# Performance work log

Measured on AMD Instinct MI355X. Metric: run time of the kernel, lower is better.

Reference implementation:

```python
import jax, jax.numpy as jnp
import numpy as np

GRID_RES_SAMPLE = 0.08  # config.grid_resolution_sample
VOXEL_SIZE = 0.04       # scene voxel size encoded in transforms


def setup_inputs() -> dict:
    key = jax.random.key(0)
    ks = jax.random.split(key, 4)
    B, X = 4, 96
    G = 192            # == ceil(X * GRID_RES_SAMPLE / VOXEL_SIZE), matches dynamic size_voxel_grid
    N = 500_000        # sparse occupied voxels per scene
    NUM_ADD = 5000     # static stand-in for occ_grids.sum()+100 mask augmentations
    # scene voxel-grid transform: scale VOXEL_SIZE, translate -5m (same structure per scene)
    T = np.eye(4, dtype=np.float32)
    T[0, 0] = T[1, 1] = T[2, 2] = VOXEL_SIZE
    T[:3, 3] = -5.0
    transforms = np.tile(T, (B, 1, 1)).astype(np.float32)
    transforms_inv = np.stack([np.linalg.inv(t) for t in transforms]).astype(np.float32)
    # per-batch regular coordinate grids with random world offsets in [0,1)m
    offs = np.asarray(jax.random.uniform(ks[0], (B, 3), dtype=jnp.float32))
    ax = np.arange(X, dtype=np.float32) * GRID_RES_SAMPLE
    gx, gy, gz = np.meshgrid(ax, ax, ax, indexing='ij')
    base = np.stack([gx, gy, gz], axis=0)  # [3,X,X,X]
    coords = (base[None] + offs[:, :, None, None, None]).astype(np.float32)
    sparse = jax.random.randint(ks[1], (B, N, 3), 0, 400, dtype=jnp.int32)
    rand_idx = jax.random.randint(ks[2], (3, NUM_ADD), 0, X, dtype=jnp.int32)
    conv_w = jnp.ones((1, 1, 5, 5, 5), jnp.float32)  # Conv3d(1,1,5) all-ones, no bias
    return {
        'coordinate_grids': jnp.asarray(coords),
        'transforms': jnp.asarray(transforms),
        'transforms_inv': jnp.asarray(transforms_inv),
        'sparse_encoding': sparse,
        'conv_w': conv_w,
        'rand_idx': rand_idx,
        'grid_size': G,
    }


def reference(coordinate_grids, transforms, transforms_inv, sparse_encoding, conv_w, rand_idx, grid_size):
    B, C, X, Y, Z = coordinate_grids.shape
    flat = coordinate_grids.reshape(B, 3, -1)
    min_loc = flat.min(-1)   # [B,3]
    max_loc = flat.max(-1)   # [B,3]
    max_size_grid = (max_loc + GRID_RES_SAMPLE - min_loc).max(0)  # [3]
    min_homo = jnp.concatenate([min_loc, jnp.ones((B, 1), flat.dtype)], axis=1)
    min_voxel_idx = jnp.floor(jnp.einsum('bij,bj->bi', transforms_inv, min_homo)[:, :3])
    min_voxel_idx = jnp.maximum(min_voxel_idx, 0.0)  # [B,3]
    size_vox = jnp.ceil(jnp.einsum('bij,j->bi', transforms_inv[:, :3, :3], max_size_grid).max(0))  # [3], == grid_size
    # shift sparse indices into the local window and filter out-of-range ones
    se = sparse_encoding.astype(jnp.float32) - min_voxel_idx[:, None, :]   # [B,N,3]
    valid = ((se >= 0) & (se < size_vox)).all(-1)                          # [B,N]
    sei = jnp.clip(se.astype(jnp.int32), 0, grid_size - 1)
    occ = jnp.zeros((B, grid_size, grid_size, grid_size), jnp.float32)
    b_idx = jnp.broadcast_to(jnp.arange(B)[:, None], valid.shape)
    occ = occ.at[b_idx, sei[..., 0], sei[..., 1], sei[..., 2]].max(valid.astype(jnp.float32))
    # world position of voxel (0,0,0) of the local window and window extent
    min_homo_idx = jnp.concatenate([min_voxel_idx, jnp.ones((B, 1), flat.dtype)], axis=1)
    pos_base = jnp.einsum('bij,bj->bi', transforms, min_homo_idx)[:, :3]   # [B,3]
    extent = jnp.einsum('bij,j->bi', transforms[:, :3, :3], size_vox)      # [B,3]
    voxel_size = extent / size_vox                                          # [B,3]
    # trilinear interpolation of dense occ grid at the coordinate grid (voxel-center convention)
    p = (coordinate_grids - pos_base[:, :, None, None, None]) / voxel_size[:, :, None, None, None] - 0.5
    p0 = jnp.floor(p)
    f = p - p0                       # [B,3,X,Y,Z]
    p0 = p0.astype(jnp.int32)
    bb = jnp.arange(B)[:, None, None, None]
    out = jnp.zeros((B, X, Y, Z), jnp.float32)
    for dx in (0, 1):
        for dy in (0, 1):
            for dz in (0, 1):
                ix = jnp.clip(p0[:, 0] + dx, 0, grid_size - 1)
                iy = jnp.clip(p0[:, 1] + dy, 0, grid_size - 1)
                iz = jnp.clip(p0[:, 2] + dz, 0, grid_size - 1)
                w = ((f[:, 0] if dx else 1 - f[:, 0]) *
                     (f[:, 1] if dy else 1 - f[:, 1]) *
                     (f[:, 2] if dz else 1 - f[:, 2]))
                out = out + w * occ[bb, ix, iy, iz]
    occ_grids = out[:, None]  # [B,1,X,Y,Z]
    # 5x5x5 all-ones conv mask
    conv = jax.lax.conv_general_dilated(
        occ_grids, conv_w, window_strides=(1, 1, 1),
        padding=[(2, 2), (2, 2), (2, 2)],
        dimension_numbers=('NCDHW', 'OIDHW', 'NCDHW'))
    mask = conv > 0
    # random-index mask augmentation (num_voxels_to_add fixed statically)
    num_add = rand_idx.shape[1]
    badd = jnp.arange(num_add) % B
    mask = mask.at[badd, 0, rand_idx[0], rand_idx[1], rand_idx[2]].set(True)
    return occ_grids.astype(bool), mask
```

## Files before the change

kernel.cpp:

```cpp
#include <hip/hip_runtime.h>
#include <math.h>

#define GS   192
#define XS   96
#define XS3  (XS*XS*XS)
#define GRS  0.08f

#define PI_OFF     256
#define PF_OFF     (256 + 1152*4)
#define OCC_OFF    16384
#define OCC_WORDS  (4*GS*GS*(GS/32))
#define OUT_OFF    (OCC_OFF + OCC_WORDS*4)
#define OUTB_WORDS (4*XS*XS*(XS/32))

__device__ __forceinline__ int clampi(int v, int lo, int hi) {
    return v < lo ? lo : (v > hi ? hi : v);
}

__global__ void k_scalars(const float* __restrict__ coords,
                          const float* __restrict__ T,
                          const float* __restrict__ Tinv,
                          float* ws, int B) {
    __shared__ int imn[12], imx[12];
    __shared__ float SS[64];
    int t = threadIdx.x;
    if (t < 12) { imn[t] = 0x7F800000; imx[t] = 0; }
    __syncthreads();
    int tot = B * 3 * XS;
    for (int e = t; e < tot; e += 256) {
        int b = e / (3 * XS); int c = (e / XS) % 3; int i = e % XS;
        size_t off = (size_t)(b*3 + c) * XS3
                   + (c == 0 ? (size_t)i * XS * XS : (c == 1 ? (size_t)i * XS : (size_t)i));
        int v = __float_as_int(coords[off]);
        atomicMin(&imn[b*3 + c], v);
        atomicMax(&imx[b*3 + c], v);
    }
    __syncthreads();
    if (t == 0) {
        float mnl[12], mxl[12];
        for (int k = 0; k < 12; k++) { mnl[k] = __int_as_float(imn[k]); mxl[k] = __int_as_float(imx[k]); }
        float msg[3];
        for (int c = 0; c < 3; c++) {
            float m = -__builtin_inff();
            for (int b = 0; b < B; b++) {
                float v = __fadd_rn(mxl[b*3 + c], GRS);
                v = __fsub_rn(v, mnl[b*3 + c]);
                m = fmaxf(m, v);
            }
            msg[c] = m;
        }
        for (int b = 0; b < B; b++)
            for (int i = 0; i < 3; i++) {
                const float* R = Tinv + b*16 + i*4;
                float v = __fmul_rn(R[0], mnl[b*3 + 0]);
                v = __fadd_rn(v, __fmul_rn(R[1], mnl[b*3 + 1]));
                v = __fadd_rn(v, __fmul_rn(R[2], mnl[b*3 + 2]));
                v = __fadd_rn(v, R[3]);
                SS[24 + b*3 + i] = fmaxf(floorf(v), 0.0f);
            }
        for (int i = 0; i < 3; i++) {
            float m = -__builtin_inff();
            for (int b = 0; b < B; b++) {
                const float* R = Tinv + b*16 + i*4;
                float v = __fmul_rn(R[0], msg[0]);
                v = __fadd_rn(v, __fmul_rn(R[1], msg[1]));
                v = __fadd_rn(v, __fmul_rn(R[2], msg[2]));
                m = fmaxf(m, v);
            }
            SS[36 + i] = ceilf(m);
        }
        for (int b = 0; b < B; b++)
            for (int i = 0; i < 3; i++) {
                const float* R = T + b*16 + i*4;
                float v = __fmul_rn(R[0], SS[24 + b*3 + 0]);
                v = __fadd_rn(v, __fmul_rn(R[1], SS[24 + b*3 + 1]));
                v = __fadd_rn(v, __fmul_rn(R[2], SS[24 + b*3 + 2]));
                v = __fadd_rn(v, R[3]);
                SS[40 + b*3 + i] = v;
            }
        for (int b = 0; b < B; b++)
            for (int i = 0; i < 3; i++) {
                const float* R = T + b*16 + i*4;
                float v = __fmul_rn(R[0], SS[36 + 0]);
                v = __fadd_rn(v, __fmul_rn(R[1], SS[36 + 1]));
                v = __fadd_rn(v, __fmul_rn(R[2], SS[36 + 2]));
                SS[52 + b*3 + i] = v / SS[36 + i];
            }
        for (int k = 24; k < 64; k++) ws[k] = SS[k];
    }
    __syncthreads();
    int* PI = (int*)((char*)ws + PI_OFF);
    float* PF = (float*)((char*)ws + PF_OFF);
    for (int e = t; e < tot; e += 256) {
        int b = e / (3 * XS); int c = (e / XS) % 3; int i = e % XS;
        size_t off = (size_t)(b*3 + c) * XS3
                   + (c == 0 ? (size_t)i * XS * XS : (c == 1 ? (size_t)i * XS : (size_t)i));
        float v = coords[off];
        float p = (v - SS[40 + b*3 + c]) / SS[52 + b*3 + c] - 0.5f;
        float p0 = floorf(p);
        PI[e] = (int)p0;
        PF[e] = p - p0;
    }
}

__global__ void k_scatter(const int* __restrict__ sparse, const float* __restrict__ ws,
                          unsigned* __restrict__ occ, int N, int total) {
    int t = blockIdx.x * blockDim.x + threadIdx.x;
    if (t >= total) return;
    int b = t / N;
    const float* S = ws;
    int s0 = sparse[(size_t)t*3 + 0];
    int s1 = sparse[(size_t)t*3 + 1];
    int s2 = sparse[(size_t)t*3 + 2];
    float e0 = (float)s0 - S[24 + b*3 + 0];
    float e1 = (float)s1 - S[24 + b*3 + 1];
    float e2 = (float)s2 - S[24 + b*3 + 2];
    if (e0 >= 0.f && e0 < S[36+0] && e1 >= 0.f && e1 < S[36+1] && e2 >= 0.f && e2 < S[36+2]) {
        int x = clampi((int)e0, 0, GS-1);
        int y = clampi((int)e1, 0, GS-1);
        int z = clampi((int)e2, 0, GS-1);
        atomicOr(&occ[(((size_t)b*GS + x)*GS + y)*(GS/32) + (z >> 5)], 1u << (z & 31));
    }
}

__global__ __launch_bounds__(256) void k_interp(const float* __restrict__ ws,
                                                const unsigned* __restrict__ occ,
                                                int* __restrict__ out0,
                                                unsigned* __restrict__ outb,
                                                int total) {
    int gid = blockIdx.x * 256 + threadIdx.x;
    if (gid >= total) return;
    int z = gid % XS;
    int r1 = gid / XS;
    int y = r1 % XS;
    int r2 = r1 / XS;
    int x = r2 % XS;
    int b = r2 / XS;
    const int* PI = (const int*)((const char*)ws + PI_OFF);
    const float* PF = (const float*)((const char*)ws + PF_OFF);
    int ix = PI[(b*3 + 0)*XS + x]; float fx = PF[(b*3 + 0)*XS + x];
    int iy = PI[(b*3 + 1)*XS + y]; float fy = PF[(b*3 + 1)*XS + y];
    int iz = PI[(b*3 + 2)*XS + z]; float fz = PF[(b*3 + 2)*XS + z];
    int x0 = clampi(ix,   0, GS-1), x1 = clampi(ix+1, 0, GS-1);
    int y0 = clampi(iy,   0, GS-1), y1 = clampi(iy+1, 0, GS-1);
    int z0 = clampi(iz,   0, GS-1), z1 = clampi(iz+1, 0, GS-1);
    float wx0 = 1.f - fx, wx1 = fx, wy0 = 1.f - fy, wy1 = fy, wz0 = 1.f - fz, wz1 = fz;
    const unsigned* r00 = occ + (((size_t)b*GS + x0)*GS + y0)*(GS/32);
    const unsigned* r01 = occ + (((size_t)b*GS + x0)*GS + y1)*(GS/32);
    const unsigned* r10 = occ + (((size_t)b*GS + x1)*GS + y0)*(GS/32);
    const unsigned* r11 = occ + (((size_t)b*GS + x1)*GS + y1)*(GS/32);
    float w00 = wx0*wy0, w01 = wx0*wy1, w10 = wx1*wy0, w11 = wx1*wy1;
    float s = 0.f;
    s += w00*wz0*(float)((r00[z0>>5] >> (z0&31)) & 1u);
    s += w00*wz1*(float)((r00[z1>>5] >> (z1&31)) & 1u);
    s += w01*wz0*(float)((r01[z0>>5] >> (z0&31)) & 1u);
    s += w01*wz1*(float)((r01[z1>>5] >> (z1&31)) & 1u);
    s += w10*wz0*(float)((r10[z0>>5] >> (z0&31)) & 1u);
    s += w10*wz1*(float)((r10[z1>>5] >> (z1&31)) & 1u);
    s += w11*wz0*(float)((r11[z0>>5] >> (z0&31)) & 1u);
    s += w11*wz1*(float)((r11[z1>>5] >> (z1&31)) & 1u);
    bool nz = (s != 0.f);
    out0[gid] = nz ? 1 : 0;
    unsigned long long m = __ballot(nz);
    int lane = threadIdx.x & 63;
    if (lane == 0)  outb[gid >> 5] = (unsigned)m;
    if (lane == 32) outb[gid >> 5] = (unsigned)(m >> 32);
}

__global__ __launch_bounds__(256) void k_dilate_bits(const unsigned* __restrict__ outb,
                                                     unsigned* __restrict__ outb2,
                                                     int totalW) {
    int t = blockIdx.x * 256 + threadIdx.x;
    if (t >= totalW) return;
    int w = t % 3;
    int r1 = t / 3;
    int j = r1 % XS;
    int r2 = r1 / XS;
    int i = r2 % XS;
    int b = r2 / XS;
    unsigned accP = 0, accC = 0, accN = 0;
    for (int di = -2; di <= 2; di++) {
        int ii = i + di; if (ii < 0 || ii >= XS) continue;
        for (int dj = -2; dj <= 2; dj++) {
            int jj = j + dj; if (jj < 0 || jj >= XS) continue;
            const unsigned* row = outb + ((size_t)(b*XS + ii)*XS + jj)*3;
            accC |= row[w];
            if (w > 0) accP |= row[w-1];
            if (w < 2) accN |= row[w+1];
        }
    }
    unsigned d = accC
               | (accC << 1) | (accP >> 31)
               | (accC << 2) | (accP >> 30)
               | (accC >> 1) | (accN << 31)
               | (accC >> 2) | (accN << 30);
    outb2[t] = d;
}

__global__ __launch_bounds__(256) void k_expand(const unsigned* __restrict__ outb2,
                                                int* __restrict__ out1, int total) {
    int gid = blockIdx.x * 256 + threadIdx.x;
    if (gid >= total) return;
    out1[gid] = (int)((outb2[gid >> 5] >> (gid & 31)) & 1u);
}

__global__ void k_rand(const int* __restrict__ rand_idx, int* __restrict__ maskout,
                       int nadd, int B) {
    int i = blockIdx.x * blockDim.x + threadIdx.x;
    if (i >= nadd) return;
    int b = i % B;
    int r0 = rand_idx[i], r1 = rand_idx[nadd + i], r2 = rand_idx[2*nadd + i];
    maskout[((size_t)(b*XS + r0)*XS + r1)*XS + r2] = 1;
}

extern "C" void kernel_launch(void* const* d_in, const int* in_sizes, int n_in,
                              void* d_out, int out_size, void* d_ws, size_t ws_size,
                              hipStream_t stream) {
    const float* coords = (const float*)d_in[0];
    const float* T      = (const float*)d_in[1];
    const float* Tinv   = (const float*)d_in[2];
    const int*   sparse = (const int*)d_in[3];
    const int*   rand_i = (const int*)d_in[5];
    int* out = (int*)d_out;

    int B = in_sizes[1] / 16;
    int N = in_sizes[3] / (B * 3);
    int nadd = in_sizes[5] / 3;

    float*    ws    = (float*)d_ws;
    unsigned* occ   = (unsigned*)((char*)d_ws + OCC_OFF);
    unsigned* outb  = (unsigned*)((char*)d_ws + OUT_OFF);
    unsigned* outb2 = (unsigned*)((char*)d_ws + OCC_OFF);
    size_t half = (size_t)B * XS3;

    hipMemsetAsync((char*)d_ws + OCC_OFF, 0, (size_t)OCC_WORDS * 4, stream);

    k_scalars<<<1, 256, 0, stream>>>(coords, T, Tinv, ws, B);
    int totalPts = B * N;
    k_scatter<<<(totalPts + 255) / 256, 256, 0, stream>>>(sparse, ws, occ, N, totalPts);
    int total = B * XS3;
    k_interp<<<(total + 255) / 256, 256, 0, stream>>>(ws, occ, out, outb, total);
    int totalW = B * XS * XS * 3;
    k_dilate_bits<<<(totalW + 255) / 256, 256, 0, stream>>>(outb, outb2, totalW);
    k_expand<<<(total + 255) / 256, 256, 0, stream>>>(outb2, out + half, total);
    k_rand<<<(nadd + 255) / 256, 256, 0, stream>>>(rand_i, out + half, nadd, B);
}
```

Baseline: 153.8 us.

## Fuse dilation, expansion and random-mask scatter into one kernel via bitmask

The random-index augmentation is now built as a bitmask by atomicOr inside the single-block scalar kernel, and that bitmask is ORed into the dilated words. Dilation and expansion to int output are fused into one kernel that stages each block's 256 words in LDS and writes its 8192 ints with a coalesced loop. This drops two kernel launches and the intermediate bit buffer round trip through global memory. In exchange the serial rand loop lands on one block, and the grid now assumes totalW is an exact multiple of 256.

New measurement: 161.1 us. +4.8%, slower.

```diff
diff --git a/kernel.cpp b/kernel.cpp
--- a/kernel.cpp
+++ b/kernel.cpp
@@ -10,8 +10,9 @@
 #define PF_OFF     (256 + 1152*4)
 #define OCC_OFF    16384
 #define OCC_WORDS  (4*GS*GS*(GS/32))
-#define OUT_OFF    (OCC_OFF + OCC_WORDS*4)
 #define OUTB_WORDS (4*XS*XS*(XS/32))
+#define RAND_OFF   (OCC_OFF + OCC_WORDS*4)
+#define OUT_OFF    (RAND_OFF + OUTB_WORDS*4)
 
 __device__ __forceinline__ int clampi(int v, int lo, int hi) {
     return v < lo ? lo : (v > hi ? hi : v);
@@ -20,10 +21,19 @@
 __global__ void k_scalars(const float* __restrict__ coords,
                           const float* __restrict__ T,
                           const float* __restrict__ Tinv,
-                          float* ws, int B) {
+                          float* ws,
+                          const int* __restrict__ rand_idx,
+                          unsigned* __restrict__ randb,
+                          int B, int nadd) {
     __shared__ int imn[12], imx[12];
     __shared__ float SS[64];
     int t = threadIdx.x;
+    for (int idx = t; idx < nadd; idx += 256) {
+        int b = idx % B;
+        int r0 = rand_idx[idx], r1 = rand_idx[nadd + idx], r2 = rand_idx[2*nadd + idx];
+        int e = ((b*XS + r0)*XS + r1)*XS + r2;
+        atomicOr(&randb[e >> 5], 1u << (e & 31));
+    }
     if (t < 12) { imn[t] = 0x7F800000; imx[t] = 0; }
     __syncthreads();
     int tot = B * 3 * XS;
@@ -167,11 +177,10 @@
     if (lane == 32) outb[gid >> 5] = (unsigned)(m >> 32);
 }
 
-__global__ __launch_bounds__(256) void k_dilate_bits(const unsigned* __restrict__ outb,
-                                                     unsigned* __restrict__ outb2,
-                                                     int totalW) {
+__global__ __launch_bounds__(256) void k_dilate_expand(const unsigned* __restrict__ outb,
+                                                       const unsigned* __restrict__ randb,
+                                                       int* __restrict__ out1) {
     int t = blockIdx.x * 256 + threadIdx.x;
-    if (t >= totalW) return;
     int w = t % 3;
     int r1 = t / 3;
     int j = r1 % XS;
@@ -194,23 +203,16 @@
                | (accC << 2) | (accP >> 30)
                | (accC >> 1) | (accN << 31)
                | (accC >> 2) | (accN << 30);
-    outb2[t] = d;
-}
-
-__global__ __launch_bounds__(256) void k_expand(const unsigned* __restrict__ outb2,
-                                                int* __restrict__ out1, int total) {
-    int gid = blockIdx.x * 256 + threadIdx.x;
-    if (gid >= total) return;
-    out1[gid] = (int)((outb2[gid >> 5] >> (gid & 31)) & 1u);
-}
-
-__global__ void k_rand(const int* __restrict__ rand_idx, int* __restrict__ maskout,
-                       int nadd, int B) {
-    int i = blockIdx.x * blockDim.x + threadIdx.x;
-    if (i >= nadd) return;
-    int b = i % B;
-    int r0 = rand_idx[i], r1 = rand_idx[nadd + i], r2 = rand_idx[2*nadd + i];
-    maskout[((size_t)(b*XS + r0)*XS + r1)*XS + r2] = 1;
+    d |= randb[t];
+    __shared__ unsigned lds[256];
+    lds[threadIdx.x] = d;
+    __syncthreads();
+    size_t base = (size_t)blockIdx.x * 8192;
+    #pragma unroll
+    for (int k = 0; k < 32; k++) {
+        int e = k * 256 + threadIdx.x;
+        out1[base + e] = (int)((lds[e >> 5] >> (e & 31)) & 1u);
+    }
 }
 
 extern "C" void kernel_launch(void* const* d_in, const int* in_sizes, int n_in,
@@ -229,19 +231,17 @@
 
     float*    ws    = (float*)d_ws;
     unsigned* occ   = (unsigned*)((char*)d_ws + OCC_OFF);
+    unsigned* randb = (unsigned*)((char*)d_ws + RAND_OFF);
     unsigned* outb  = (unsigned*)((char*)d_ws + OUT_OFF);
-    unsigned* outb2 = (unsigned*)((char*)d_ws + OCC_OFF);
     size_t half = (size_t)B * XS3;
 
-    hipMemsetAsync((char*)d_ws + OCC_OFF, 0, (size_t)OCC_WORDS * 4, stream);
-
-    k_scalars<<<1, 256, 0, stream>>>(coords, T, Tinv, ws, B);
+    hipMemsetAsync((char*)d_ws + OCC_OFF, 0, (size_t)(OCC_WORDS + OUTB_WORDS) * 4, stream);
+
+    k_scalars<<<1, 256, 0, stream>>>(coords, T, Tinv, ws, rand_i, randb, B, nadd);
     int totalPts = B * N;
     k_scatter<<<(totalPts + 255) / 256, 256, 0, stream>>>(sparse, ws, occ, N, totalPts);
     int total = B * XS3;
     k_interp<<<(total + 255) / 256, 256, 0, stream>>>(ws, occ, out, outb, total);
     int totalW = B * XS * XS * 3;
-    k_dilate_bits<<<(totalW + 255) / 256, 256, 0, stream>>>(outb, outb2, totalW);
-    k_expand<<<(total + 255) / 256, 256, 0, stream>>>(outb2, out + half, total);
-    k_rand<<<(nadd + 255) / 256, 256, 0, stream>>>(rand_i, out + half, nadd, B);
-}
+    k_dilate_expand<<<totalW / 256, 256, 0, stream>>>(outb, randb, out + half);
+}
```
